# Optimization experiments

Measured on AMD Instinct MI355X. Metric: run time of the kernel, lower is better.

The kernel has to match this reference:

```python
import jax, jax.numpy as jnp
import numpy as np

B, N, IN_F, OUT_F, OP_D = 64, 96, 128, 128, 48
SKIP_IDX = 1
ATTN_SCALE = 1.0


def setup_inputs() -> dict:
    key = jax.random.key(0)
    ks = jax.random.split(key, 7)
    return {
        "inputs": jax.random.normal(ks[0], (B, N, IN_F), dtype=jnp.float32),
        "adj": jax.random.randint(ks[1], (B, N, N), 0, 5, dtype=jnp.int64),
        "op_emb": jax.random.normal(ks[2], (B, N, N, OP_D), dtype=jnp.float32),
        "weight": jax.random.normal(ks[3], (IN_F, OUT_F), dtype=jnp.float32) * (1.0 / np.sqrt(OUT_F)),
        "attn_w": jax.random.normal(ks[4], (OP_D, OUT_F), dtype=jnp.float32) * (1.0 / np.sqrt(OP_D)),
        "attn_b": jax.random.normal(ks[5], (OUT_F,), dtype=jnp.float32) * 0.01,
        "self_op_emb": jax.random.normal(ks[6], (OP_D,), dtype=jnp.float32),
    }


def reference(inputs, adj, op_emb, weight, attn_w, attn_b, self_op_emb):
    # support: [B, N, OUT_F]
    support = jnp.matmul(inputs, weight)
    n = adj.shape[-1]
    eye = jnp.eye(n, dtype=bool)  # [N, N]
    # plus_I: replace diagonal op embeddings with self_op_emb, add I to adj
    op_emb = jnp.where(eye[..., None], self_op_emb, op_emb)  # [B,N,N,OP_D]
    adj = adj + eye.astype(adj.dtype)
    # attention over op embeddings: [B,N,N,OUT_F]
    attn = jax.nn.sigmoid(jnp.matmul(op_emb, attn_w) + attn_b)
    attn = (adj != 0)[..., None].astype(attn.dtype) * attn * ATTN_SCALE
    # skip-connection edges get attention == 1
    is_skip = (adj == SKIP_IDX)[..., None].astype(attn.dtype)
    attn = is_skip + (1.0 - is_skip) * attn
    # processed_info = sum_j attn[b,i,j,:] * support[b,j,:]; residual = support
    processed_info = jnp.einsum("bijd,bjd->bid", attn, support)
    return processed_info + support
```

## Files before the change

kernel.cpp:

```cpp
#include <hip/hip_runtime.h>
#include <hip/hip_bf16.h>


#define B_ 64
#define N_ 96
#define F_ 128
#define D_ 48
#define G_ 12
#define NGRP (N_ / G_)

typedef __attribute__((ext_vector_type(8))) short short8;
typedef __attribute__((ext_vector_type(4))) float f32x4;

#if __has_builtin(__builtin_amdgcn_exp2f)
#define EXP2(x) __builtin_amdgcn_exp2f(x)
#else
#define EXP2(x) exp2f(x)
#endif

__device__ __forceinline__ void gload_lds16(const void* g, void* l) {
    __builtin_amdgcn_global_load_lds(
        (const __attribute__((address_space(1))) void*)g,
        (__attribute__((address_space(3))) void*)l, 16, 0, 0);
}

__device__ __forceinline__ size_t s2i(int b, int mt, int r, int lg, int fbp) {
    return ((((size_t)b * 6 + mt) * 4 + r) * 4 + lg) * 64 + fbp;
}

__device__ __forceinline__ unsigned bfbits(float x) {
    union { __hip_bfloat16 h; unsigned short u; } cv;
    cv.h = __float2bfloat16(x);
    return (unsigned)cv.u;
}

__global__ __launch_bounds__(256, 4) void support_kernel(
    const float* __restrict__ inputs, const float* __restrict__ weight,
    float2* __restrict__ S2)
{
    __shared__ float in_lds[16 * F_];
    const int tid = threadIdx.x;
    const int row0 = blockIdx.x * 16;
    ((float4*)in_lds)[tid]       = ((const float4*)(inputs + (size_t)row0 * F_))[tid];
    ((float4*)in_lds)[tid + 256] = ((const float4*)(inputs + (size_t)row0 * F_))[tid + 256];
    __syncthreads();
    const int rl = tid >> 4, f0 = (tid & 15) * 8;
    float acc[8] = {0.f,0.f,0.f,0.f,0.f,0.f,0.f,0.f};
    #pragma unroll 4
    for (int k = 0; k < F_; ++k) {
        const float a = in_lds[rl * F_ + k];
        const float4 w0 = *(const float4*)(weight + k * F_ + f0);
        const float4 w1 = *(const float4*)(weight + k * F_ + f0 + 4);
        acc[0] += a * w0.x; acc[1] += a * w0.y; acc[2] += a * w0.z; acc[3] += a * w0.w;
        acc[4] += a * w1.x; acc[5] += a * w1.y; acc[6] += a * w1.z; acc[7] += a * w1.w;
    }
    const int R = row0 + rl;
    const int b = R / N_, j = R - b * N_;
    const int mt = j >> 4, lg = (j >> 2) & 3, r = j & 3;
    #pragma unroll
    for (int q = 0; q < 4; ++q) {
        const int fbp = (f0 >> 1) + q;
        S2[s2i(b, mt, r, lg, fbp)] = make_float2(acc[2 * q], acc[2 * q + 1]);
    }
}

__global__ __launch_bounds__(512, 4) void fused_kernel(
    const float* __restrict__ op_emb,
    const unsigned* __restrict__ adjw,
    const float* __restrict__ attn_w,
    const float* __restrict__ attn_b,
    const float* __restrict__ self_op,
    const float2* __restrict__ S2,
    float* __restrict__ out)
{
    __shared__ __align__(16) float F32buf[3][N_ * D_];
    __shared__ __align__(16) unsigned short Atile[2][N_ * 64];
    __shared__ __align__(8)  float2 Ppart[2][4][16];

    const int tid  = threadIdx.x;
    const int lane = tid & 63;
    const int wid  = tid >> 6;
    const int wf   = wid & 3;
    const int wj   = wid >> 2;
    const int lg   = lane >> 4;
    const int lm   = lane & 15;
    const int fb   = wf * 32 + lm * 2;
    const int fbp  = wf * 16 + lm;

    const int blk = blockIdx.x;
    const int b   = blk / NGRP;
    const int grp = blk - b * NGRP;
    const int i0  = grp * G_;

    const float kNL2E = -1.44269504088896f;

    const unsigned probe = adjw[2 * lane + 1];
    const bool use32 = __any(probe != 0);

    auto issue_tile = [&](int i, int pb) {
        const char* gbase = (const char*)(op_emb + (size_t)(b * N_ + i) * N_ * D_);
        char* lbase = (char*)(&F32buf[pb][0]);
        #pragma unroll
        for (int c0 = 0; c0 < 3; ++c0) {
            int c = wid + 8 * c0;
            c = (c < 18) ? c : 17;
            gload_lds16(gbase + c * 1024 + lane * 16, lbase + c * 1024);
        }
    };

    issue_tile(i0, 0);
    issue_tile(i0 + 1, 1);

    unsigned mcode = 0;
    if (tid < N_) {
        #pragma unroll
        for (int g2 = 0; g2 < G_; ++g2) {
            const size_t idx = (size_t)(b * N_ + i0 + g2) * N_ + tid;
            int a = use32 ? (int)adjw[idx] : (int)adjw[2 * idx];
            a += (tid == i0 + g2) ? 1 : 0;
            const unsigned code = (a == 0) ? 0u : ((a == 1) ? 1u : 2u);
            mcode |= code << (2 * g2);
        }
    }

    short8 bfrag[2][2];
    float  bbias[2];
    {
        const float2 bb = *(const float2*)(attn_b + fb);
        bbias[0] = bb.x * kNL2E;
        bbias[1] = bb.y * kNL2E;
        #pragma unroll
        for (int ks = 0; ks < 2; ++ks) {
            short8 v0, v1;
            #pragma unroll
            for (int e = 0; e < 8; ++e) {
                const int d = ks * 32 + lg * 8 + e;
                if (d < D_) {
                    const float2 w = *(const float2*)(attn_w + d * F_ + fb);
                    v0[e] = (short)bfbits(w.x * kNL2E);
                    v1[e] = (short)bfbits(w.y * kNL2E);
                } else {
                    const unsigned one = (d == D_) ? bfbits(1.0f) : 0u;
                    v0[e] = (short)one;
                    v1[e] = (short)one;
                }
            }
            bfrag[0][ks] = v0;
            bfrag[1][ks] = v1;
        }
    }

    float2 sfrag[3][4];
    #pragma unroll
    for (int s = 0; s < 3; ++s)
        #pragma unroll
        for (int r = 0; r < 4; ++r)
            sfrag[s][r] = S2[s2i(b, 3 * wj + s, r, lg, fbp)];

    for (int v = tid; v < 2 * N_ * 7; v += 512) {
        const int t = v / (N_ * 7);
        const int vv = v - t * (N_ * 7);
        const int j = vv / 7, q = vv - 7 * j;
        const int byte = j * 128 + ((100 + q * 4) ^ ((j & 7) << 4));
        *(unsigned*)((char*)(&Atile[t][0]) + byte) = 0u;
    }

    __syncthreads();

    auto convert_tile = [&](int gg) {
        const int ic = i0 + gg;
        const float* fsrc = &F32buf[gg % 3][0];
        #pragma unroll
        for (int s = 0; s < 3; ++s) {
            const int w = tid + s * 512;
            if (w < N_ * 12) {
                const int j = w / 12, c = w - 12 * j;
                float4 p;
                if (j == ic) p = *(const float4*)(self_op + c * 4);
                else         p = *(const float4*)((const char*)fsrc + 16 * w);
                const int byte = j * 128 + ((c * 8) ^ ((j & 7) << 4));
                *(uint2*)((char*)(&Atile[gg & 1][0]) + byte) =
                    make_uint2(bfbits(p.x) | (bfbits(p.y) << 16),
                               bfbits(p.z) | (bfbits(p.w) << 16));
            }
        }
        if (tid < N_) {
            const unsigned code = (mcode >> (2 * gg)) & 3u;
            const unsigned bits = (code == 0) ? 0x42FCu : ((code == 1) ? 0xC2FCu : 0u);
            const int byte = tid * 128 + (96 ^ ((tid & 7) << 4));
            *(unsigned*)((char*)(&Atile[gg & 1][0]) + byte) = bits;
        }
    };

    convert_tile(0);
    asm volatile("s_waitcnt lgkmcnt(0)" ::: "memory");
    __builtin_amdgcn_s_barrier();

    float osum_prev0 = 0.f, osum_prev1 = 0.f;

    #pragma unroll 1
    for (int g = 0; g < G_; ++g) {
        const int i = i0 + g;

        if (wj == 0 && lg == 0) {
            const int ip = (g > 0) ? (i - 1) : i0;
            const float2 srv = S2[s2i(b, ip >> 4, ip & 3, (ip >> 2) & 3, fbp)];
            if (g > 0) {
                const float2 pp = Ppart[(g - 1) & 1][wf][lm];
                float2 o;
                o.x = osum_prev0 + pp.x + srv.x;
                o.y = osum_prev1 + pp.y + srv.y;
                *(float2*)(out + (size_t)(b * N_ + ip) * F_ + fb) = o;
            }
        }

        {
            const int inx = (g + 2 < G_) ? (g + 2) : (G_ - 1);
            issue_tile(i0 + inx, (g + 2) % 3);
        }

        if (wj == 0) asm volatile("s_waitcnt vmcnt(4)" ::: "memory");
        else         asm volatile("s_waitcnt vmcnt(3)" ::: "memory");

        convert_tile(g + 1);

        float osum0 = 0.f, osum1 = 0.f;
        #pragma unroll
        for (int s = 0; s < 3; ++s) {
            const int mt  = 3 * wj + s;
            const int jr  = mt * 16 + lm;
            const int swz = (lm & 7) << 4;
            const char* base = (const char*)(&Atile[g & 1][0]) + jr * 128;
            const short8 a0 = *(const short8*)(base + (( 0 + lg * 16) ^ swz));
            const short8 a1 = *(const short8*)(base + ((64 + lg * 16) ^ swz));
            f32x4 c0 = (f32x4){bbias[0], bbias[0], bbias[0], bbias[0]};
            f32x4 c1 = (f32x4){bbias[1], bbias[1], bbias[1], bbias[1]};
            c0 = __builtin_amdgcn_mfma_f32_16x16x32_bf16(a0, bfrag[0][0], c0, 0, 0, 0);
            c0 = __builtin_amdgcn_mfma_f32_16x16x32_bf16(a1, bfrag[0][1], c0, 0, 0, 0);
            c1 = __builtin_amdgcn_mfma_f32_16x16x32_bf16(a0, bfrag[1][0], c1, 0, 0, 0);
            c1 = __builtin_amdgcn_mfma_f32_16x16x32_bf16(a1, bfrag[1][1], c1, 0, 0, 0);
            #pragma unroll
            for (int r = 0; r < 4; ++r) {
                const float s0 = __builtin_amdgcn_rcpf(1.f + EXP2(c0[r]));
                const float s1 = __builtin_amdgcn_rcpf(1.f + EXP2(c1[r]));
                osum0 = __builtin_fmaf(s0, sfrag[s][r].x, osum0);
                osum1 = __builtin_fmaf(s1, sfrag[s][r].y, osum1);
            }
        }
        osum0 += __shfl_xor(osum0, 16);
        osum0 += __shfl_xor(osum0, 32);
        osum1 += __shfl_xor(osum1, 16);
        osum1 += __shfl_xor(osum1, 32);
        if (wj == 1 && lg == 0)
            Ppart[g & 1][wf][lm] = make_float2(osum0, osum1);
        osum_prev0 = osum0;
        osum_prev1 = osum1;

        asm volatile("s_waitcnt lgkmcnt(0)" ::: "memory");
        __builtin_amdgcn_s_barrier();
    }

    if (wj == 0 && lg == 0) {
        const int ip = i0 + G_ - 1;
        const float2 pp = Ppart[(G_ - 1) & 1][wf][lm];
        const float2 sr = S2[s2i(b, ip >> 4, ip & 3, (ip >> 2) & 3, fbp)];
        float2 o;
        o.x = osum_prev0 + pp.x + sr.x;
        o.y = osum_prev1 + pp.y + sr.y;
        *(float2*)(out + (size_t)(b * N_ + ip) * F_ + fb) = o;
    }
}

extern "C" void kernel_launch(void* const* d_in, const int* in_sizes, int n_in,
                              void* d_out, int out_size, void* d_ws, size_t ws_size,
                              hipStream_t stream) {
    const float*    inputs  = (const float*)d_in[0];
    const unsigned* adjw    = (const unsigned*)d_in[1];
    const float*    op_emb  = (const float*)d_in[2];
    const float*    weight  = (const float*)d_in[3];
    const float*    attn_w  = (const float*)d_in[4];
    const float*    attn_b  = (const float*)d_in[5];
    const float*    self_op = (const float*)d_in[6];
    float* out = (float*)d_out;
    float2* S2 = (float2*)d_ws;

    support_kernel<<<(B_ * N_) / 16, 256, 0, stream>>>(inputs, weight, S2);
    fused_kernel<<<B_ * NGRP, 512, 0, stream>>>(op_emb, adjw, attn_w, attn_b, self_op,
                                                S2, out);
}
```

Measured before the change: 59.75 us.

## Software-pipeline MFMA results one row ahead of sigmoid epilogue

Restructures the per-row loop so each iteration issues the MFMAs for row g into a ping-pong accumulator set and runs the sigmoid/weighted-sum epilogue on the previous row's accumulators. The loop is unrolled by two, and output writes are delayed by two iterations. The aim is to hide MFMA latency behind transcendental math. Per-thread address offsets for the convert and LDS reads are also hoisted out of the loop. In exchange it holds more accumulator registers and adds a drain stage after the loop.

Measured after the change: 71.96 us. 20.4% more time.

```diff
diff --git a/kernel.cpp b/kernel.cpp
--- a/kernel.cpp
+++ b/kernel.cpp
@@ -157,6 +157,29 @@
         for (int r = 0; r < 4; ++r)
             sfrag[s][r] = S2[s2i(b, 3 * wj + s, r, lg, fbp)];
 
+    int cvj[3], crd[3], cwb[3];
+    bool cvalid[3];
+    #pragma unroll
+    for (int s = 0; s < 3; ++s) {
+        const int w = tid + s * 512;
+        cvalid[s] = (w < N_ * 12);
+        const int j = w / 12, c = w - 12 * j;
+        cvj[s] = j;
+        crd[s] = 16 * w;
+        cwb[s] = j * 128 + ((c * 8) ^ ((j & 7) << 4));
+    }
+    const int selfrd[3] = { (tid % 12) * 16, ((tid + 512) % 12) * 16, ((tid + 1024) % 12) * 16 };
+    const int maskbyte = tid * 128 + (96 ^ ((tid & 7) << 4));
+
+    int a0off[3], a1off[3];
+    #pragma unroll
+    for (int s = 0; s < 3; ++s) {
+        const int jr  = (3 * wj + s) * 16 + lm;
+        const int swz = (lm & 7) << 4;
+        a0off[s] = jr * 128 + (( 0 + lg * 16) ^ swz);
+        a1off[s] = jr * 128 + ((64 + lg * 16) ^ swz);
+    }
+
     for (int v = tid; v < 2 * N_ * 7; v += 512) {
         const int t = v / (N_ * 7);
         const int vv = v - t * (N_ * 7);
@@ -167,19 +190,16 @@
 
     __syncthreads();
 
-    auto convert_tile = [&](int gg) {
+    auto convert_tile = [&](int gg, unsigned short* atile_nxt) {
         const int ic = i0 + gg;
         const float* fsrc = &F32buf[gg % 3][0];
         #pragma unroll
         for (int s = 0; s < 3; ++s) {
-            const int w = tid + s * 512;
-            if (w < N_ * 12) {
-                const int j = w / 12, c = w - 12 * j;
+            if (cvalid[s]) {
                 float4 p;
-                if (j == ic) p = *(const float4*)(self_op + c * 4);
-                else         p = *(const float4*)((const char*)fsrc + 16 * w);
-                const int byte = j * 128 + ((c * 8) ^ ((j & 7) << 4));
-                *(uint2*)((char*)(&Atile[gg & 1][0]) + byte) =
+                if (cvj[s] == ic) p = *(const float4*)((const char*)self_op + selfrd[s]);
+                else              p = *(const float4*)((const char*)fsrc + crd[s]);
+                *(uint2*)((char*)atile_nxt + cwb[s]) =
                     make_uint2(bfbits(p.x) | (bfbits(p.y) << 16),
                                bfbits(p.z) | (bfbits(p.w) << 16));
             }
@@ -187,29 +207,29 @@
         if (tid < N_) {
             const unsigned code = (mcode >> (2 * gg)) & 3u;
             const unsigned bits = (code == 0) ? 0x42FCu : ((code == 1) ? 0xC2FCu : 0u);
-            const int byte = tid * 128 + (96 ^ ((tid & 7) << 4));
-            *(unsigned*)((char*)(&Atile[gg & 1][0]) + byte) = bits;
+            *(unsigned*)((char*)atile_nxt + maskbyte) = bits;
         }
     };
 
-    convert_tile(0);
+    convert_tile(0, &Atile[0][0]);
     asm volatile("s_waitcnt lgkmcnt(0)" ::: "memory");
     __builtin_amdgcn_s_barrier();
 
-    float osum_prev0 = 0.f, osum_prev1 = 0.f;
-
-    #pragma unroll 1
-    for (int g = 0; g < G_; ++g) {
+    f32x4 accA[3][2], accB[3][2];
+    float osum_sv0 = 0.f, osum_sv1 = 0.f;
+
+    auto body = [&](int g, f32x4 (*accW)[2], f32x4 (*accR)[2],
+                    const unsigned short* atile_cur, unsigned short* atile_nxt) {
         const int i = i0 + g;
 
         if (wj == 0 && lg == 0) {
-            const int ip = (g > 0) ? (i - 1) : i0;
+            const int ip = (g >= 2) ? (i - 2) : i0;
             const float2 srv = S2[s2i(b, ip >> 4, ip & 3, (ip >> 2) & 3, fbp)];
-            if (g > 0) {
-                const float2 pp = Ppart[(g - 1) & 1][wf][lm];
+            if (g >= 2) {
+                const float2 pp = Ppart[g & 1][wf][lm];
                 float2 o;
-                o.x = osum_prev0 + pp.x + srv.x;
-                o.y = osum_prev1 + pp.y + srv.y;
+                o.x = osum_sv0 + pp.x + srv.x;
+                o.y = osum_sv1 + pp.y + srv.y;
                 *(float2*)(out + (size_t)(b * N_ + ip) * F_ + fb) = o;
             }
         }
@@ -222,27 +242,71 @@
         if (wj == 0) asm volatile("s_waitcnt vmcnt(4)" ::: "memory");
         else         asm volatile("s_waitcnt vmcnt(3)" ::: "memory");
 
-        convert_tile(g + 1);
-
-        float osum0 = 0.f, osum1 = 0.f;
+        if (g + 1 < G_) convert_tile(g + 1, atile_nxt);
+
         #pragma unroll
         for (int s = 0; s < 3; ++s) {
-            const int mt  = 3 * wj + s;
-            const int jr  = mt * 16 + lm;
-            const int swz = (lm & 7) << 4;
-            const char* base = (const char*)(&Atile[g & 1][0]) + jr * 128;
-            const short8 a0 = *(const short8*)(base + (( 0 + lg * 16) ^ swz));
-            const short8 a1 = *(const short8*)(base + ((64 + lg * 16) ^ swz));
+            const short8 a0 = *(const short8*)((const char*)atile_cur + a0off[s]);
+            const short8 a1 = *(const short8*)((const char*)atile_cur + a1off[s]);
             f32x4 c0 = (f32x4){bbias[0], bbias[0], bbias[0], bbias[0]};
             f32x4 c1 = (f32x4){bbias[1], bbias[1], bbias[1], bbias[1]};
             c0 = __builtin_amdgcn_mfma_f32_16x16x32_bf16(a0, bfrag[0][0], c0, 0, 0, 0);
             c0 = __builtin_amdgcn_mfma_f32_16x16x32_bf16(a1, bfrag[0][1], c0, 0, 0, 0);
             c1 = __builtin_amdgcn_mfma_f32_16x16x32_bf16(a0, bfrag[1][0], c1, 0, 0, 0);
             c1 = __builtin_amdgcn_mfma_f32_16x16x32_bf16(a1, bfrag[1][1], c1, 0, 0, 0);
+            accW[s][0] = c0;
+            accW[s][1] = c1;
+        }
+
+        if (g >= 1) {
+            float osum0 = 0.f, osum1 = 0.f;
+            #pragma unroll
+            for (int s = 0; s < 3; ++s) {
+                #pragma unroll
+                for (int r = 0; r < 4; ++r) {
+                    const float s0 = __builtin_amdgcn_rcpf(1.f + EXP2(accR[s][0][r]));
+                    const float s1 = __builtin_amdgcn_rcpf(1.f + EXP2(accR[s][1][r]));
+                    osum0 = __builtin_fmaf(s0, sfrag[s][r].x, osum0);
+                    osum1 = __builtin_fmaf(s1, sfrag[s][r].y, osum1);
+                }
+            }
+            osum0 += __shfl_xor(osum0, 16);
+            osum0 += __shfl_xor(osum0, 32);
+            osum1 += __shfl_xor(osum1, 16);
+            osum1 += __shfl_xor(osum1, 32);
+            if (wj == 1 && lg == 0)
+                Ppart[(g - 1) & 1][wf][lm] = make_float2(osum0, osum1);
+            osum_sv0 = osum0;
+            osum_sv1 = osum1;
+        }
+
+        asm volatile("s_waitcnt lgkmcnt(0)" ::: "memory");
+        __builtin_amdgcn_s_barrier();
+    };
+
+    #pragma unroll 1
+    for (int gp = 0; gp < G_; gp += 2) {
+        body(gp,     accA, accB, &Atile[0][0], &Atile[1][0]);
+        body(gp + 1, accB, accA, &Atile[1][0], &Atile[0][0]);
+    }
+
+    if (wj == 0 && lg == 0) {
+        const int ip = i0 + G_ - 2;
+        const float2 pp = Ppart[(G_ - 2) & 1][wf][lm];
+        const float2 sr = S2[s2i(b, ip >> 4, ip & 3, (ip >> 2) & 3, fbp)];
+        float2 o;
+        o.x = osum_sv0 + pp.x + sr.x;
+        o.y = osum_sv1 + pp.y + sr.y;
+        *(float2*)(out + (size_t)(b * N_ + ip) * F_ + fb) = o;
+    }
+    {
+        float osum0 = 0.f, osum1 = 0.f;
+        #pragma unroll
+        for (int s = 0; s < 3; ++s) {
             #pragma unroll
             for (int r = 0; r < 4; ++r) {
-                const float s0 = __builtin_amdgcn_rcpf(1.f + EXP2(c0[r]));
-                const float s1 = __builtin_amdgcn_rcpf(1.f + EXP2(c1[r]));
+                const float s0 = __builtin_amdgcn_rcpf(1.f + EXP2(accB[s][0][r]));
+                const float s1 = __builtin_amdgcn_rcpf(1.f + EXP2(accB[s][1][r]));
                 osum0 = __builtin_fmaf(s0, sfrag[s][r].x, osum0);
                 osum1 = __builtin_fmaf(s1, sfrag[s][r].y, osum1);
             }
@@ -252,22 +316,18 @@
         osum1 += __shfl_xor(osum1, 16);
         osum1 += __shfl_xor(osum1, 32);
         if (wj == 1 && lg == 0)
-            Ppart[g & 1][wf][lm] = make_float2(osum0, osum1);
-        osum_prev0 = osum0;
-        osum_prev1 = osum1;
-
+            Ppart[(G_ - 1) & 1][wf][lm] = make_float2(osum0, osum1);
         asm volatile("s_waitcnt lgkmcnt(0)" ::: "memory");
         __builtin_amdgcn_s_barrier();
-    }
-
-    if (wj == 0 && lg == 0) {
-        const int ip = i0 + G_ - 1;
-        const float2 pp = Ppart[(G_ - 1) & 1][wf][lm];
-        const float2 sr = S2[s2i(b, ip >> 4, ip & 3, (ip >> 2) & 3, fbp)];
-        float2 o;
-        o.x = osum_prev0 + pp.x + sr.x;
-        o.y = osum_prev1 + pp.y + sr.y;
-        *(float2*)(out + (size_t)(b * N_ + ip) * F_ + fb) = o;
+        if (wj == 0 && lg == 0) {
+            const int ip = i0 + G_ - 1;
+            const float2 pp = Ppart[(G_ - 1) & 1][wf][lm];
+            const float2 sr = S2[s2i(b, ip >> 4, ip & 3, (ip >> 2) & 3, fbp)];
+            float2 o;
+            o.x = osum0 + pp.x + sr.x;
+            o.y = osum1 + pp.y + sr.y;
+            *(float2*)(out + (size_t)(b * N_ + ip) * F_ + fb) = o;
+        }
     }
 }
 
```
